# Kernel optimization log

Measured on AMD Instinct MI355X. Metric: run time of the kernel, lower is better.

Reference implementation:

```python
import jax, jax.numpy as jnp
import numpy as np

N, L, S, C, H = 4, 2048, 4096, 256, 8
D = C // H          # head dim = 32
HID = 4 * C         # mlp hidden = 1024
LN_EPS = 1e-5
LA_EPS = 1e-6


def _layer_norm(x, g, b):
    m = x.mean(-1, keepdims=True)
    v = ((x - m) ** 2).mean(-1, keepdims=True)
    return (x - m) * jax.lax.rsqrt(v + LN_EPS) * g + b


def _linear_attention(q, k, v):
    # q: [N,L,H,D], k/v: [N,S,H,D]  (elu feature map linear attention)
    Q = jax.nn.elu(q) + 1.0
    K = jax.nn.elu(k) + 1.0
    v_len = v.shape[1]
    KV = jnp.einsum('nshd,nshv->nhdv', K, v / v_len)
    Z = 1.0 / (jnp.einsum('nlhd,nhd->nlh', Q, K.sum(axis=1)) + LA_EPS)
    return jnp.einsum('nlhd,nhdv,nlh->nlhv', Q, KV, Z) * v_len


def setup_inputs() -> dict:
    key = jax.random.key(0)
    ks = jax.random.split(key, 32)
    f32 = jnp.float32
    w = lambda k, *s: (jax.random.normal(k, s, dtype=f32) * 0.02)
    inp = {
        'tgt': jax.random.normal(ks[0], (N, L, C), dtype=f32),
        'memory': jax.random.normal(ks[1], (N, S, C), dtype=f32),
        'tgt_pos': jax.random.normal(ks[2], (N, L, C), dtype=f32),
        'pos_embed': w(ks[3], 1, S, C),
        # layer norms
        'ln1_g': jnp.ones((C,), f32), 'ln1_b': jnp.zeros((C,), f32),
        'ln2_g': jnp.ones((C,), f32), 'ln2_b': jnp.zeros((C,), f32),
        'ln3_g': jnp.ones((C,), f32), 'ln3_b': jnp.zeros((C,), f32),
        # self-attn projections (stored (in,out))
        'wq': w(ks[4], C, C), 'bq': jnp.zeros((C,), f32),
        'wk': w(ks[5], C, C), 'bk': jnp.zeros((C,), f32),
        'wv': w(ks[6], C, C), 'bv': jnp.zeros((C,), f32),
        'w_merge': w(ks[7], C, C),
        # cross-attn (CCAttention) projections
        'cwq': w(ks[8], C, C), 'cbq': jnp.zeros((C,), f32),
        'cwk': w(ks[9], C, C), 'cbk': jnp.zeros((C,), f32),
        'cwv': w(ks[10], C, C), 'cbv': jnp.zeros((C,), f32),
        'cwo': w(ks[11], C, C), 'cbo': jnp.zeros((C,), f32),
        # mlp (fc1 -> dwconv3x3 -> gelu -> fc2)
        'mw1': w(ks[12], C, HID), 'mb1': jnp.zeros((HID,), f32),
        'dw_k': w(ks[13], HID, 1, 3, 3), 'dw_b': jnp.zeros((HID,), f32),
        'mw2': w(ks[14], HID, C), 'mb2': jnp.zeros((C,), f32),
        'num_points': L,
    }
    return inp


def reference(tgt, memory, tgt_pos, pos_embed,
              ln1_g, ln1_b, ln2_g, ln2_b, ln3_g, ln3_b,
              wq, bq, wk, bk, wv, bv, w_merge,
              cwq, cbq, cwk, cbk, cwv, cbv, cwo, cbo,
              mw1, mb1, dw_k, dw_b, mw2, mb2, num_points):
    n, l, c = tgt.shape
    # ---- self attention (linear attention) ----
    tgt2 = _layer_norm(tgt, ln1_g, ln1_b)
    qk = tgt2 + tgt_pos
    q = (qk @ wq + bq).reshape(n, l, H, D)
    k = (qk @ wk + bk).reshape(n, l, H, D)
    v = (tgt2 @ wv + bv).reshape(n, l, H, D)
    msg = _linear_attention(q, k, v).reshape(n, l, c) @ w_merge
    tgt = tgt + msg  # dropout is identity in eval
    # ---- cross attention (CCAttention, softmax MHA) ----
    tgt2 = _layer_norm(tgt, ln2_g, ln2_b)
    mem = memory + pos_embed
    cq = (tgt2 @ cwq + cbq).reshape(n, l, H, D)
    ck = (mem @ cwk + cbk).reshape(n, -1, H, D)
    cv = (mem @ cwv + cbv).reshape(n, -1, H, D)
    scale = D ** -0.5
    attn = jax.nn.softmax(jnp.einsum('nlhd,nshd->nhls', cq, ck) * scale, axis=-1)
    cmsg = jnp.einsum('nhls,nshd->nlhd', attn, cv).reshape(n, l, c) @ cwo + cbo
    tgt = tgt + cmsg
    # ---- MLP with depthwise conv over (num_points, 1) grid ----
    x = _layer_norm(tgt, ln3_g, ln3_b)
    h = x @ mw1 + mb1                                   # [n,l,HID]
    hi = h.transpose(0, 2, 1).reshape(n, HID, num_points, 1)
    hi = jax.lax.conv_general_dilated(
        hi, dw_k, window_strides=(1, 1), padding=((1, 1), (1, 1)),
        feature_group_count=HID,
        dimension_numbers=('NCHW', 'OIHW', 'NCHW'))
    hi = hi + dw_b[None, :, None, None]
    h = hi.reshape(n, HID, l).transpose(0, 2, 1)
    h = jax.nn.gelu(h, approximate=False)
    mlp_out = h @ mw2 + mb2
    return tgt + mlp_out
```

## Files before the change

### kernel.cpp

```cpp
#include <hip/hip_runtime.h>
#include <hip/hip_bf16.h>
#include <math.h>

#define NB 4
#define LL 2048
#define SS 4096
#define CC 256
#define HH 8
#define DD 32
#define HIDN 1024
#define NSPLIT 2

using bf16 = __hip_bfloat16;
typedef __attribute__((ext_vector_type(8))) short short8;
typedef __attribute__((ext_vector_type(4))) short short4v;
typedef __attribute__((ext_vector_type(4))) float floatx4;

__device__ __forceinline__ float b2f(bf16 x) { return __bfloat162float(x); }
__device__ __forceinline__ short f2bs(float x) {
    bf16 h = __float2bfloat16(x);
    return *(short*)&h;
}
__device__ __forceinline__ short f2bs_fast(float x) {
    return (short)(__float_as_uint(x) >> 16);
}
__device__ __forceinline__ float s2f(short s) {
    bf16 h = *(bf16*)&s;
    return __bfloat162float(h);
}

#if __has_builtin(__builtin_amdgcn_exp2f)
#define EXP2(x) __builtin_amdgcn_exp2f(x)
#else
#define EXP2(x) exp2f(x)
#endif

__device__ __forceinline__ bool probe_f32(const unsigned* p) {
    return p[0] == 0x3F800000u;
}
__device__ __forceinline__ float ldx(const void* p, size_t i, bool f32m) {
    return f32m ? ((const float*)p)[i] : b2f(((const bf16*)p)[i]);
}

__global__ __launch_bounds__(256)
void zero_kernel(float* __restrict__ p, int n) {
    int i = blockIdx.x * 256 + threadIdx.x;
    if (i < n) p[i] = 0.0f;
}

struct WPack { const void* p[10]; };

__global__ __launch_bounds__(256)
void wprep_kernel(WPack pk, short* __restrict__ dst,
                  const unsigned* __restrict__ probe) {
    const bool f32m = probe_f32(probe);
    const int z = blockIdx.z;
    const int K = (z == 9) ? 1024 : 256;
    const int N = (z == 8) ? 1024 : 256;
    const size_t off = (z < 8) ? (size_t)z * 65536 : (z == 8 ? 524288u : 786432u);
    const int k0 = blockIdx.y * 64, n0 = blockIdx.x * 64;
    if (k0 >= K || n0 >= N) return;
    __shared__ float T[64][65];
    const void* src = pk.p[z];
    const int tid = threadIdx.x;
    #pragma unroll
    for (int p = 0; p < 16; ++p) {
        int idx = tid + p * 256;
        int r = idx >> 6, c = idx & 63;
        T[r][c] = ldx(src, (size_t)(k0 + r) * N + n0 + c, f32m);
    }
    __syncthreads();
    short* d = dst + off;
    #pragma unroll
    for (int p = 0; p < 16; ++p) {
        int idx = tid + p * 256;
        int c2 = idx >> 6, r2 = idx & 63;
        d[(size_t)(n0 + c2) * K + k0 + r2] = f2bs(T[r2][c2]);
    }
}

__global__ __launch_bounds__(256)
void ln_kernel(const void* __restrict__ xr, const float* __restrict__ xf,
               const void* __restrict__ g, const void* __restrict__ bta,
               const void* __restrict__ pos,
               short* __restrict__ y, short* __restrict__ y2,
               const unsigned* __restrict__ probe) {
    const bool f32m = probe_f32(probe);
    const int row = blockIdx.x;
    const int c = threadIdx.x;
    const size_t base = (size_t)row * CC;
    float x = xr ? ldx(xr, base + c, f32m) : xf[base + c];
    float a = x, b = x * x;
    #pragma unroll
    for (int off = 32; off; off >>= 1) {
        a += __shfl_down(a, off);
        b += __shfl_down(b, off);
    }
    __shared__ float sa[4], sb[4];
    if ((c & 63) == 0) { sa[c >> 6] = a; sb[c >> 6] = b; }
    __syncthreads();
    float s1 = sa[0] + sa[1] + sa[2] + sa[3];
    float s2 = sb[0] + sb[1] + sb[2] + sb[3];
    float mean = s1 * (1.0f / CC);
    float var = s2 * (1.0f / CC) - mean * mean;
    float inv = rsqrtf(var + 1e-5f);
    float yv = (x - mean) * inv * ldx(g, c, f32m) + ldx(bta, c, f32m);
    y[base + c] = f2bs(yv);
    if (y2) y2[base + c] = f2bs(yv + ldx(pos, base + c, f32m));
}

__global__ __launch_bounds__(256)
void addpos_kernel(const void* __restrict__ mem, const void* __restrict__ pos,
                   short* __restrict__ out, const unsigned* __restrict__ probe) {
    const bool f32m = probe_f32(probe);
    const int row = blockIdx.x;
    const int c = threadIdx.x;
    const int s = row & (SS - 1);
    out[(size_t)row * CC + c] =
        f2bs(ldx(mem, (size_t)row * CC + c, f32m) + ldx(pos, (size_t)s * CC + c, f32m));
}

template <int BM, int BN, int EPI, int OUTMODE, int TRANSC2>
__global__ __launch_bounds__(256)
void gemm_mfma_kernel(const short* __restrict__ A, const short* __restrict__ Bt,
                      const void* __restrict__ bias, const void* __restrict__ bias2,
                      const float* __restrict__ residF, const void* __restrict__ residR,
                      void* __restrict__ Cout, void* __restrict__ Cout2,
                      int M, int N, int K, const unsigned* __restrict__ probe) {
    const bool f32m = probe_f32(probe);
    constexpr int WM = BM / 2, AI = WM / 16;
    constexpr int WN = BN / 2, BJ = WN / 16;
    constexpr int ACH = (BM == 128) ? 4 : 2;
    constexpr int BCH = (BN == 128) ? 4 : 2;
    __shared__ __attribute__((aligned(16))) short As[BM][72];
    __shared__ __attribute__((aligned(16))) short Bs[BN][72];
    const int tid = threadIdx.x;
    const int ln = tid & 15, quad = (tid >> 4) & 3, w = tid >> 6;
    const int wm = (w & 1) * WM, wn = (w >> 1) * WN;
    const int bm = blockIdx.y * BM, bn = blockIdx.x * BN;
    const int ar = (BM == 128) ? (tid >> 1) : (tid >> 2);
    const int ac = (BM == 128) ? ((tid & 1) * 32) : ((tid & 3) * 16);
    const int br = (BN == 128) ? (tid >> 1) : (tid >> 2);
    const int bc = (BN == 128) ? ((tid & 1) * 32) : ((tid & 3) * 16);

    short8 pa[ACH], pb[BCH];
    {
        const short* ag = &A[(size_t)(bm + ar) * K + ac];
        #pragma unroll
        for (int t = 0; t < ACH; ++t) pa[t] = *(const short8*)(ag + t * 8);
        const short* bg = &Bt[(size_t)(bn + br) * K + bc];
        #pragma unroll
        for (int t = 0; t < BCH; ++t) pb[t] = *(const short8*)(bg + t * 8);
    }
    floatx4 acc[AI][BJ] = {};
    for (int k0 = 0; k0 < K; k0 += 64) {
        #pragma unroll
        for (int t = 0; t < ACH; ++t) *(short8*)&As[ar][ac + t * 8] = pa[t];
        #pragma unroll
        for (int t = 0; t < BCH; ++t) *(short8*)&Bs[br][bc + t * 8] = pb[t];
        if (k0 + 64 < K) {
            const short* ag = &A[(size_t)(bm + ar) * K + k0 + 64 + ac];
            #pragma unroll
            for (int t = 0; t < ACH; ++t) pa[t] = *(const short8*)(ag + t * 8);
            const short* bg = &Bt[(size_t)(bn + br) * K + k0 + 64 + bc];
            #pragma unroll
            for (int t = 0; t < BCH; ++t) pb[t] = *(const short8*)(bg + t * 8);
        }
        __syncthreads();
        #pragma unroll
        for (int ks = 0; ks < 2; ++ks) {
            short8 af[AI], bf[BJ];
            #pragma unroll
            for (int i = 0; i < AI; ++i)
                af[i] = *(const short8*)&As[wm + i * 16 + ln][ks * 32 + quad * 8];
            #pragma unroll
            for (int j = 0; j < BJ; ++j)
                bf[j] = *(const short8*)&Bs[wn + j * 16 + ln][ks * 32 + quad * 8];
            #pragma unroll
            for (int i = 0; i < AI; ++i)
                #pragma unroll
                for (int j = 0; j < BJ; ++j)
                    acc[i][j] = __builtin_amdgcn_mfma_f32_16x16x32_bf16(af[i], bf[j], acc[i][j], 0, 0, 0);
        }
        __syncthreads();
    }
    #pragma unroll
    for (int i = 0; i < AI; ++i)
        #pragma unroll
        for (int j = 0; j < BJ; ++j) {
            const int gr0 = bm + wm + i * 16 + quad * 4;
            const int gc = bn + wn + j * 16 + ln;
            const bool hi = (Cout2 != nullptr) && (gc >= 256);
            const int col = hi ? gc - 256 : gc;
            const int sN = Cout2 ? 256 : N;
            void* co = hi ? Cout2 : Cout;
            const void* bb = hi ? bias2 : bias;
            float vv[4];
            #pragma unroll
            for (int r = 0; r < 4; ++r) {
                float v = acc[i][j][r];
                if (bb) v += ldx(bb, col, f32m);
                if (EPI == 1) v = (v > 0.0f) ? (v + 1.0f) : __expf(v);
                const size_t o = (size_t)(gr0 + r) * sN + col;
                if (residF) v += residF[o];
                if (residR) v += ldx(residR, o, f32m);
                vv[r] = v;
            }
            if (TRANSC2 && hi) {
                const int nb = gr0 >> 12;
                const int s = gr0 & (SS - 1);
                short4v pk4 = {f2bs(vv[0]), f2bs(vv[1]), f2bs(vv[2]), f2bs(vv[3])};
                *(short4v*)&((short*)co)[((size_t)nb * CC + col) * SS + s] = pk4;
            } else {
                #pragma unroll
                for (int r = 0; r < 4; ++r) {
                    const size_t o = (size_t)(gr0 + r) * sN + col;
                    if (OUTMODE == 0) ((float*)co)[o] = vv[r];
                    else if (OUTMODE == 2) ((short*)co)[o] = f2bs(vv[r]);
                    else {
                        if (f32m) ((float*)co)[o] = vv[r];
                        else      ((bf16*)co)[o] = __float2bfloat16(vv[r]);
                    }
                }
            }
        }
}

#define KVSPLIT 16
__global__ __launch_bounds__(256)
void linattn_kv_kernel(const float* __restrict__ Kp, const float* __restrict__ Vp,
                       float* __restrict__ KV, float* __restrict__ Ksum) {
    const int h = blockIdx.x, n = blockIdx.y, z = blockIdx.z;
    __shared__ __attribute__((aligned(16))) float Kt[64][33];
    __shared__ __attribute__((aligned(16))) float Vt[64][32];
    const int tid = threadIdx.x;
    const int d = tid >> 3, e0 = (tid & 7) * 4;
    const int sbeg = z * (LL / KVSPLIT), send = sbeg + (LL / KVSPLIT);
    float acc[4] = {}, ks = 0.0f;
    for (int s0 = sbeg; s0 < send; s0 += 64) {
        #pragma unroll
        for (int p = 0; p < 8; ++p) {
            int idx = tid + p * 256;
            int r = idx >> 5, c = idx & 31;
            size_t gaddr = (size_t)((n * LL) + s0 + r) * CC + h * DD + c;
            Kt[r][c] = Kp[gaddr];
            Vt[r][c] = Vp[gaddr];
        }
        __syncthreads();
        for (int s = 0; s < 64; ++s) {
            float kd = Kt[s][d];
            ks += kd;
            float4 v4 = *(const float4*)&Vt[s][e0];
            acc[0] += kd * v4.x; acc[1] += kd * v4.y;
            acc[2] += kd * v4.z; acc[3] += kd * v4.w;
        }
        __syncthreads();
    }
    float* kvp = &KV[(size_t)((n * HH + h) * DD + d) * DD + e0];
    atomicAdd(&kvp[0], acc[0]); atomicAdd(&kvp[1], acc[1]);
    atomicAdd(&kvp[2], acc[2]); atomicAdd(&kvp[3], acc[3]);
    if ((tid & 7) == 0) atomicAdd(&Ksum[(n * HH + h) * DD + d], ks);
}

__global__ __launch_bounds__(256)
void linattn_out_kernel(const float* __restrict__ Qp, const float* __restrict__ KV,
                        const float* __restrict__ Ksum, short* __restrict__ Out) {
    const int lt = blockIdx.x, h = blockIdx.y, n = blockIdx.z;
    __shared__ float KVs[32][33];
    __shared__ float Ks[32];
    __shared__ float Qs[64][33];
    const int tid = threadIdx.x;
    for (int p = 0; p < 4; ++p) {
        int idx = tid + p * 256;
        KVs[idx >> 5][idx & 31] = KV[(size_t)(n * HH + h) * (DD * DD) + idx];
    }
    if (tid < 32) Ks[tid] = Ksum[(n * HH + h) * DD + tid];
    for (int p = 0; p < 8; ++p) {
        int idx = tid + p * 256;
        int r = idx >> 5, c = idx & 31;
        Qs[r][c] = Qp[(size_t)((n * LL) + lt * 64 + r) * CC + h * DD + c];
    }
    __syncthreads();
    const int e = tid & 31;
    for (int ii = 0; ii < 8; ++ii) {
        const int i = (tid >> 5) + ii * 8;
        float num = 0.0f, den = 0.0f;
        for (int d = 0; d < 32; ++d) {
            float q = Qs[i][d];
            num += q * KVs[d][e];
            den += q * Ks[d];
        }
        Out[(size_t)((n * LL) + lt * 64 + i) * CC + h * DD + e] = f2bs(num / (den + 1e-6f));
    }
}

__global__ __launch_bounds__(256)
void flash_mfma_kernel(const short* __restrict__ Q, const short* __restrict__ K,
                       const short* __restrict__ V,
                       float* __restrict__ Of, float* __restrict__ Lp) {
    const int lt = blockIdx.x, h = blockIdx.y;
    const int n = blockIdx.z >> 1, sp = blockIdx.z & 1;
    const int tid = threadIdx.x;
    const int ln = tid & 15;
    const int quad = (tid >> 4) & 3;
    const int w = tid >> 6;
    const int NT = NB * LL;
    const float qscale = 0.17677669529663687f * 1.4426950408889634f;

    __shared__ __attribute__((aligned(16))) short Qs[64][40];
    __shared__ __attribute__((aligned(16))) short Ks[2][64][40];
    __shared__ __attribute__((aligned(16))) short Vp[2][32][72];

    {
        const int r = tid >> 2, c0 = (tid & 3) * 8;
        short8 qv = *(const short8*)&Q[(size_t)((n * LL) + lt * 64 + r) * CC + h * DD + c0];
        short tmp[8];
        #pragma unroll
        for (int j = 0; j < 8; ++j) tmp[j] = f2bs(s2f(qv[j]) * qscale);
        *(short8*)&Qs[r][c0] = *(short8*)tmp;
    }
    __syncthreads();

    short8 bQ = *(const short8*)&Qs[w * 16 + ln][quad * 8];

    const short one_b = (short)0x3F80;
    const short8 ones8 = {one_b, one_b, one_b, one_b, one_b, one_b, one_b, one_b};

    floatx4 o0 = {0.f, 0.f, 0.f, 0.f};
    floatx4 o1 = {0.f, 0.f, 0.f, 0.f};
    floatx4 o2 = {0.f, 0.f, 0.f, 0.f};
    const floatx4 zinit = {-24.f, -24.f, -24.f, -24.f};

    const int r_st = tid >> 2, c0_st = (tid & 3) * 8;
    const int e_st = tid >> 3, m_st = tid & 7;
    const int K32 = (m_st >> 2) * 32;
    const int h4 = ((m_st >> 1) & 1) * 4;
    const int q0s = (2 * m_st) & 3;
    const int slotA = K32 + q0s * 8 + h4;
    const int slotB = K32 + (q0s + 1) * 8 + h4;

    const int sbeg = sp * (SS / NSPLIT);
    constexpr int NIT = (SS / NSPLIT) / 64;

    const short* kptr = &K[(size_t)((n * SS) + sbeg + r_st) * CC + h * DD + c0_st];
    const short* vptr = &V[((size_t)n * CC + h * DD + e_st) * SS + sbeg + m_st * 8];
    short8 kreg = *(const short8*)kptr;
    short8 vreg = *(const short8*)vptr;

    for (int it = 0; it < NIT; ++it) {
        const int buf = it & 1;
        *(short8*)&Ks[buf][r_st][c0_st] = kreg;
        {
            short4v lo = {vreg[0], vreg[1], vreg[2], vreg[3]};
            short4v hi = {vreg[4], vreg[5], vreg[6], vreg[7]};
            *(short4v*)&Vp[buf][e_st][slotA] = lo;
            *(short4v*)&Vp[buf][e_st][slotB] = hi;
        }
        if (it + 1 < NIT) {
            kreg = *(const short8*)(kptr + (size_t)(it + 1) * 64 * CC);
            vreg = *(const short8*)(vptr + (it + 1) * 64);
        }
        __syncthreads();

        floatx4 sc[4];
        #pragma unroll
        for (int g = 0; g < 4; ++g) {
            short8 aK = *(const short8*)&Ks[buf][g * 16 + ln][quad * 8];
            sc[g] = __builtin_amdgcn_mfma_f32_16x16x32_bf16(aK, bQ, zinit, 0, 0, 0);
        }

        #pragma unroll
        for (int ks = 0; ks < 2; ++ks) {
            union { unsigned u[4]; short8 s8; } cvt;
            #pragma unroll
            for (int jj = 0; jj < 4; ++jj) {
                const int j0 = 2 * jj, j1 = 2 * jj + 1;
                float p0 = EXP2(sc[2 * ks + (j0 >> 2)][j0 & 3]);
                float p1 = EXP2(sc[2 * ks + (j1 >> 2)][j1 & 3]);
                cvt.u[jj] = __builtin_amdgcn_perm(
                    __float_as_uint(p1), __float_as_uint(p0), 0x07060302u);
            }
            short8 aP = cvt.s8;
            short8 bV0 = *(const short8*)&Vp[buf][ln][ks * 32 + quad * 8];
            short8 bV1 = *(const short8*)&Vp[buf][16 + ln][ks * 32 + quad * 8];
            o0 = __builtin_amdgcn_mfma_f32_16x16x32_bf16(aP, bV0, o0, 0, 0, 0);
            o1 = __builtin_amdgcn_mfma_f32_16x16x32_bf16(aP, bV1, o1, 0, 0, 0);
            o2 = __builtin_amdgcn_mfma_f32_16x16x32_bf16(aP, ones8, o2, 0, 0, 0);
        }
    }

    const int rowbase = lt * 64 + w * 16;
    if (ln == 0) {
        #pragma unroll
        for (int r = 0; r < 4; ++r)
            Lp[((size_t)sp * NT + (size_t)n * LL + rowbase + quad * 4 + r) * HH + h] = o2[r];
    }
    #pragma unroll
    for (int r = 0; r < 4; ++r) {
        const size_t row = (size_t)n * LL + rowbase + quad * 4 + r;
        float* o = &Of[((size_t)sp * NT + row) * CC + h * DD];
        o[ln] = o0[r];
        o[16 + ln] = o1[r];
    }
}

__global__ __launch_bounds__(256)
void flash_merge_kernel(const float* __restrict__ Of, const float* __restrict__ Lp,
                        short* __restrict__ O) {
    const int row = blockIdx.x, c = threadIdx.x, h = c >> 5;
    const size_t NT = (size_t)NB * LL;
    float l = Lp[(size_t)row * HH + h] + Lp[(NT + row) * HH + h];
    float v = Of[(size_t)row * CC + c] + Of[NT * CC + (size_t)row * CC + c];
    O[(size_t)row * CC + c] = f2bs(v / l);
}

__global__ __launch_bounds__(256)
void dwconv_gelu_kernel(const short* __restrict__ H1, const void* __restrict__ wk,
                        const void* __restrict__ wb, short* __restrict__ H2,
                        const unsigned* __restrict__ probe) {
    const bool f32m = probe_f32(probe);
    const int row = blockIdx.x;
    const int l = row & (LL - 1);
    const int c0 = threadIdx.x * 4;
    const short* cur = &H1[(size_t)row * HIDN + c0];
    short4v xc = *(const short4v*)cur;
    short4v xm = {}, xp = {};
    if (l > 0)      xm = *(const short4v*)(cur - HIDN);
    if (l < LL - 1) xp = *(const short4v*)(cur + HIDN);
    short r[4];
    #pragma unroll
    for (int j = 0; j < 4; ++j) {
        int ch = c0 + j;
        float wm = ldx(wk, ch * 9 + 1, f32m);
        float w0 = ldx(wk, ch * 9 + 4, f32m);
        float wp = ldx(wk, ch * 9 + 7, f32m);
        float v = s2f(xm[j]) * wm + s2f(xc[j]) * w0 + s2f(xp[j]) * wp + ldx(wb, ch, f32m);
        r[j] = f2bs(0.5f * v * (1.0f + erff(v * 0.70710678118654752f)));
    }
    short4v out = {r[0], r[1], r[2], r[3]};
    *(short4v*)&H2[(size_t)row * HIDN + c0] = out;
}

extern "C" void kernel_launch(void* const* d_in, const int* in_sizes, int n_in,
                              void* d_out, int out_size, void* d_ws, size_t ws_size,
                              hipStream_t stream) {
    const void* tgt      = d_in[0];
    const void* memory   = d_in[1];
    const void* tgt_pos  = d_in[2];
    const void* pos_emb  = d_in[3];
    const void* ln1_g = d_in[4],  *ln1_b = d_in[5];
    const void* ln2_g = d_in[6],  *ln2_b = d_in[7];
    const void* ln3_g = d_in[8],  *ln3_b = d_in[9];
    const void* wq = d_in[10], *bq = d_in[11];
    const void* wk = d_in[12], *bk = d_in[13];
    const void* wv = d_in[14], *bv = d_in[15];
    const void* w_merge = d_in[16];
    const void* cwq = d_in[17], *cbq = d_in[18];
    const void* cwk = d_in[19], *cbk = d_in[20];
    const void* cwv = d_in[21], *cbv = d_in[22];
    const void* cwo = d_in[23], *cbo = d_in[24];
    const void* mw1 = d_in[25], *mb1 = d_in[26];
    const void* dw_k = d_in[27], *dw_b = d_in[28];
    const void* mw2 = d_in[29], *mb2 = d_in[30];
    const unsigned* probe = (const unsigned*)d_in[4];

    char* w = (char*)d_ws;
    const size_t MB = 1024 * 1024;
    short* lnout_b = (short*)(w + 0 * MB);
    short* qk_b    = (short*)(w + 4 * MB);
    float* Tbuf    = (float*)(w + 8 * MB);
    float* phiq    = (float*)(w + 16 * MB);
    float* phik    = (float*)(w + 24 * MB);
    float* vbuf    = (float*)(w + 32 * MB);
    float* KVb     = (float*)(w + 40 * MB);
    float* Ksb     = (float*)(w + 40 * MB + 131072);
    short* cqbuf   = (short*)(w + 41 * MB);
    short* membuf  = (short*)(w + 45 * MB);
    short* ckbuf   = (short*)(w + 53 * MB);
    short* cvT     = (short*)(w + 69 * MB);
    short* flashO  = (short*)(w + 77 * MB);
    short* wT      = (short*)(w + 81 * MB);
    float* Ofb     = (float*)(w + 16 * MB);
    float* Lpb     = (float*)(w + 32 * MB);
    short* H1      = (short*)(w + 16 * MB);
    short* H2      = (short*)(w + 32 * MB);

    short* wqT  = wT + 0 * 65536;
    short* wvT  = wT + 2 * 65536;
    short* wmT  = wT + 3 * 65536;
    short* cwqT = wT + 4 * 65536;
    short* cwkT = wT + 5 * 65536;
    short* cwoT = wT + 7 * 65536;
    short* mw1T = wT + 524288;
    short* mw2T = wT + 786432;

    const int NT = NB * LL;
    const int NS = NB * SS;
    const dim3 blk(256);

    WPack pk;
    pk.p[0] = wq;  pk.p[1] = wk;  pk.p[2] = wv;  pk.p[3] = w_merge;
    pk.p[4] = cwq; pk.p[5] = cwk; pk.p[6] = cwv; pk.p[7] = cwo;
    pk.p[8] = mw1; pk.p[9] = mw2;
    wprep_kernel<<<dim3(16, 16, 10), blk, 0, stream>>>(pk, wT, probe);
    zero_kernel<<<dim3(137), blk, 0, stream>>>(KVb, 35072);

    ln_kernel<<<NT, blk, 0, stream>>>(tgt, nullptr, ln1_g, ln1_b, tgt_pos, lnout_b, qk_b, probe);
    gemm_mfma_kernel<64, 64, 1, 0, 0><<<dim3(8, NT / 64), blk, 0, stream>>>(
        qk_b, wqT, bq, bk, nullptr, nullptr, phiq, phik, NT, 512, CC, probe);
    gemm_mfma_kernel<64, 64, 0, 0, 0><<<dim3(4, NT / 64), blk, 0, stream>>>(
        lnout_b, wvT, bv, nullptr, nullptr, nullptr, vbuf, nullptr, NT, CC, CC, probe);
    linattn_kv_kernel<<<dim3(HH, NB, KVSPLIT), blk, 0, stream>>>(phik, vbuf, KVb, Ksb);
    linattn_out_kernel<<<dim3(LL / 64, HH, NB), blk, 0, stream>>>(phiq, KVb, Ksb, (short*)vbuf);
    gemm_mfma_kernel<64, 64, 0, 0, 0><<<dim3(4, NT / 64), blk, 0, stream>>>(
        (short*)vbuf, wmT, nullptr, nullptr, nullptr, tgt, Tbuf, nullptr, NT, CC, CC, probe);

    ln_kernel<<<NT, blk, 0, stream>>>(nullptr, Tbuf, ln2_g, ln2_b, nullptr, lnout_b, nullptr, probe);
    addpos_kernel<<<NS, blk, 0, stream>>>(memory, pos_emb, membuf, probe);
    gemm_mfma_kernel<64, 64, 0, 2, 0><<<dim3(4, NT / 64), blk, 0, stream>>>(
        lnout_b, cwqT, cbq, nullptr, nullptr, nullptr, cqbuf, nullptr, NT, CC, CC, probe);
    gemm_mfma_kernel<64, 64, 0, 2, 1><<<dim3(8, NS / 64), blk, 0, stream>>>(
        membuf, cwkT, cbk, cbv, nullptr, nullptr, ckbuf, cvT, NS, 512, CC, probe);
    flash_mfma_kernel<<<dim3(LL / 64, HH, NB * NSPLIT), blk, 0, stream>>>(
        cqbuf, ckbuf, cvT, Ofb, Lpb);
    flash_merge_kernel<<<NT, blk, 0, stream>>>(Ofb, Lpb, flashO);
    gemm_mfma_kernel<64, 64, 0, 0, 0><<<dim3(4, NT / 64), blk, 0, stream>>>(
        flashO, cwoT, cbo, nullptr, Tbuf, nullptr, Tbuf, nullptr, NT, CC, CC, probe);

    ln_kernel<<<NT, blk, 0, stream>>>(nullptr, Tbuf, ln3_g, ln3_b, nullptr, lnout_b, nullptr, probe);
    gemm_mfma_kernel<64, 64, 0, 2, 0><<<dim3(16, NT / 64), blk, 0, stream>>>(
        lnout_b, mw1T, mb1, nullptr, nullptr, nullptr, H1, nullptr, NT, HIDN, CC, probe);
    dwconv_gelu_kernel<<<NT, blk, 0, stream>>>(H1, dw_k, dw_b, H2, probe);
    gemm_mfma_kernel<64, 64, 0, 1, 0><<<dim3(4, NT / 64), blk, 0, stream>>>(
        H2, mw2T, mb2, nullptr, Tbuf, nullptr, d_out, nullptr, NT, CC, HIDN, probe);

    (void)in_sizes; (void)n_in; (void)out_size; (void)ws_size;
}
```

Measured before the change: 428.7 us.

## Process 128 query rows per flash block and fold zeroing into wprep

The cross-attention flash kernel now handles two 64-row query tiles per block. Each K/V tile loaded into shared memory is reused for twice as many queries, which halves global K/V traffic and barrier count per query row. The grid shrinks to 16x8x8=1024 blocks, and register pressure rises from the doubled accumulators and score tiles. Separately, the KV buffer zeroing launch is merged into the weight-prep kernel as an extra z-slice, removing one kernel launch.

```diff
diff --git a/kernel.cpp b/kernel.cpp
--- a/kernel.cpp
+++ b/kernel.cpp
@@ -42,19 +42,19 @@
     return f32m ? ((const float*)p)[i] : b2f(((const bf16*)p)[i]);
 }
 
-__global__ __launch_bounds__(256)
-void zero_kernel(float* __restrict__ p, int n) {
-    int i = blockIdx.x * 256 + threadIdx.x;
-    if (i < n) p[i] = 0.0f;
-}
-
 struct WPack { const void* p[10]; };
 
 __global__ __launch_bounds__(256)
-void wprep_kernel(WPack pk, short* __restrict__ dst,
+void wprep_kernel(WPack pk, short* __restrict__ dst, float* __restrict__ zbuf,
                   const unsigned* __restrict__ probe) {
+    const int z = blockIdx.z;
+    const int tid = threadIdx.x;
+    if (z == 10) {
+        int idx = (blockIdx.y * 16 + blockIdx.x) * 256 + tid;
+        if (idx < 35072) zbuf[idx] = 0.0f;
+        return;
+    }
     const bool f32m = probe_f32(probe);
-    const int z = blockIdx.z;
     const int K = (z == 9) ? 1024 : 256;
     const int N = (z == 8) ? 1024 : 256;
     const size_t off = (z < 8) ? (size_t)z * 65536 : (z == 8 ? 524288u : 786432u);
@@ -62,7 +62,6 @@
     if (k0 >= K || n0 >= N) return;
     __shared__ float T[64][65];
     const void* src = pk.p[z];
-    const int tid = threadIdx.x;
     #pragma unroll
     for (int p = 0; p < 16; ++p) {
         int idx = tid + p * 256;
@@ -307,28 +306,34 @@
     const int NT = NB * LL;
     const float qscale = 0.17677669529663687f * 1.4426950408889634f;
 
-    __shared__ __attribute__((aligned(16))) short Qs[64][40];
+    __shared__ __attribute__((aligned(16))) short Qs[128][40];
     __shared__ __attribute__((aligned(16))) short Ks[2][64][40];
     __shared__ __attribute__((aligned(16))) short Vp[2][32][72];
 
     {
         const int r = tid >> 2, c0 = (tid & 3) * 8;
-        short8 qv = *(const short8*)&Q[(size_t)((n * LL) + lt * 64 + r) * CC + h * DD + c0];
-        short tmp[8];
-        #pragma unroll
-        for (int j = 0; j < 8; ++j) tmp[j] = f2bs(s2f(qv[j]) * qscale);
-        *(short8*)&Qs[r][c0] = *(short8*)tmp;
+        #pragma unroll
+        for (int hf = 0; hf < 2; ++hf) {
+            short8 qv = *(const short8*)
+                &Q[(size_t)((n * LL) + lt * 128 + hf * 64 + r) * CC + h * DD + c0];
+            short tmp[8];
+            #pragma unroll
+            for (int j = 0; j < 8; ++j) tmp[j] = f2bs(s2f(qv[j]) * qscale);
+            *(short8*)&Qs[hf * 64 + r][c0] = *(short8*)tmp;
+        }
     }
     __syncthreads();
 
-    short8 bQ = *(const short8*)&Qs[w * 16 + ln][quad * 8];
+    short8 bQa = *(const short8*)&Qs[w * 16 + ln][quad * 8];
+    short8 bQb = *(const short8*)&Qs[64 + w * 16 + ln][quad * 8];
 
     const short one_b = (short)0x3F80;
     const short8 ones8 = {one_b, one_b, one_b, one_b, one_b, one_b, one_b, one_b};
 
-    floatx4 o0 = {0.f, 0.f, 0.f, 0.f};
-    floatx4 o1 = {0.f, 0.f, 0.f, 0.f};
-    floatx4 o2 = {0.f, 0.f, 0.f, 0.f};
+    floatx4 o0a = {0.f, 0.f, 0.f, 0.f}, o1a = {0.f, 0.f, 0.f, 0.f};
+    floatx4 o2a = {0.f, 0.f, 0.f, 0.f};
+    floatx4 o0b = {0.f, 0.f, 0.f, 0.f}, o1b = {0.f, 0.f, 0.f, 0.f};
+    floatx4 o2b = {0.f, 0.f, 0.f, 0.f};
     const floatx4 zinit = {-24.f, -24.f, -24.f, -24.f};
 
     const int r_st = tid >> 2, c0_st = (tid & 3) * 8;
@@ -362,45 +367,63 @@
         }
         __syncthreads();
 
-        floatx4 sc[4];
+        floatx4 sa[4], sb[4];
         #pragma unroll
         for (int g = 0; g < 4; ++g) {
             short8 aK = *(const short8*)&Ks[buf][g * 16 + ln][quad * 8];
-            sc[g] = __builtin_amdgcn_mfma_f32_16x16x32_bf16(aK, bQ, zinit, 0, 0, 0);
+            sa[g] = __builtin_amdgcn_mfma_f32_16x16x32_bf16(aK, bQa, zinit, 0, 0, 0);
+            sb[g] = __builtin_amdgcn_mfma_f32_16x16x32_bf16(aK, bQb, zinit, 0, 0, 0);
         }
 
         #pragma unroll
         for (int ks = 0; ks < 2; ++ks) {
-            union { unsigned u[4]; short8 s8; } cvt;
+            union { unsigned u[4]; short8 s8; } ca, cb;
             #pragma unroll
             for (int jj = 0; jj < 4; ++jj) {
                 const int j0 = 2 * jj, j1 = 2 * jj + 1;
-                float p0 = EXP2(sc[2 * ks + (j0 >> 2)][j0 & 3]);
-                float p1 = EXP2(sc[2 * ks + (j1 >> 2)][j1 & 3]);
-                cvt.u[jj] = __builtin_amdgcn_perm(
-                    __float_as_uint(p1), __float_as_uint(p0), 0x07060302u);
+                float pa0 = EXP2(sa[2 * ks + (j0 >> 2)][j0 & 3]);
+                float pa1 = EXP2(sa[2 * ks + (j1 >> 2)][j1 & 3]);
+                ca.u[jj] = __builtin_amdgcn_perm(
+                    __float_as_uint(pa1), __float_as_uint(pa0), 0x07060302u);
+                float pb0 = EXP2(sb[2 * ks + (j0 >> 2)][j0 & 3]);
+                float pb1 = EXP2(sb[2 * ks + (j1 >> 2)][j1 & 3]);
+                cb.u[jj] = __builtin_amdgcn_perm(
+                    __float_as_uint(pb1), __float_as_uint(pb0), 0x07060302u);
             }
-            short8 aP = cvt.s8;
             short8 bV0 = *(const short8*)&Vp[buf][ln][ks * 32 + quad * 8];
             short8 bV1 = *(const short8*)&Vp[buf][16 + ln][ks * 32 + quad * 8];
-            o0 = __builtin_amdgcn_mfma_f32_16x16x32_bf16(aP, bV0, o0, 0, 0, 0);
-            o1 = __builtin_amdgcn_mfma_f32_16x16x32_bf16(aP, bV1, o1, 0, 0, 0);
-            o2 = __builtin_amdgcn_mfma_f32_16x16x32_bf16(aP, ones8, o2, 0, 0, 0);
-        }
-    }
-
-    const int rowbase = lt * 64 + w * 16;
+            o0a = __builtin_amdgcn_mfma_f32_16x16x32_bf16(ca.s8, bV0, o0a, 0, 0, 0);
+            o1a = __builtin_amdgcn_mfma_f32_16x16x32_bf16(ca.s8, bV1, o1a, 0, 0, 0);
+            o2a = __builtin_amdgcn_mfma_f32_16x16x32_bf16(ca.s8, ones8, o2a, 0, 0, 0);
+            o0b = __builtin_amdgcn_mfma_f32_16x16x32_bf16(cb.s8, bV0, o0b, 0, 0, 0);
+            o1b = __builtin_amdgcn_mfma_f32_16x16x32_bf16(cb.s8, bV1, o1b, 0, 0, 0);
+            o2b = __builtin_amdgcn_mfma_f32_16x16x32_bf16(cb.s8, ones8, o2b, 0, 0, 0);
+        }
+    }
+
+    const int rb_a = lt * 128 + w * 16;
+    const int rb_b = rb_a + 64;
     if (ln == 0) {
         #pragma unroll
-        for (int r = 0; r < 4; ++r)
-            Lp[((size_t)sp * NT + (size_t)n * LL + rowbase + quad * 4 + r) * HH + h] = o2[r];
+        for (int r = 0; r < 4; ++r) {
+            Lp[((size_t)sp * NT + (size_t)n * LL + rb_a + quad * 4 + r) * HH + h] = o2a[r];
+            Lp[((size_t)sp * NT + (size_t)n * LL + rb_b + quad * 4 + r) * HH + h] = o2b[r];
+        }
     }
     #pragma unroll
     for (int r = 0; r < 4; ++r) {
-        const size_t row = (size_t)n * LL + rowbase + quad * 4 + r;
-        float* o = &Of[((size_t)sp * NT + row) * CC + h * DD];
-        o[ln] = o0[r];
-        o[16 + ln] = o1[r];
+        {
+            const size_t row = (size_t)n * LL + rb_a + quad * 4 + r;
+            float* o = &Of[((size_t)sp * NT + row) * CC + h * DD];
+            o[ln] = o0a[r];
+            o[16 + ln] = o1a[r];
+        }
+        {
+            const size_t row = (size_t)n * LL + rb_b + quad * 4 + r;
+            float* o = &Of[((size_t)sp * NT + row) * CC + h * DD];
+            o[ln] = o0b[r];
+            o[16 + ln] = o1b[r];
+        }
     }
 }
 
@@ -502,8 +525,7 @@
     pk.p[0] = wq;  pk.p[1] = wk;  pk.p[2] = wv;  pk.p[3] = w_merge;
     pk.p[4] = cwq; pk.p[5] = cwk; pk.p[6] = cwv; pk.p[7] = cwo;
     pk.p[8] = mw1; pk.p[9] = mw2;
-    wprep_kernel<<<dim3(16, 16, 10), blk, 0, stream>>>(pk, wT, probe);
-    zero_kernel<<<dim3(137), blk, 0, stream>>>(KVb, 35072);
+    wprep_kernel<<<dim3(16, 16, 11), blk, 0, stream>>>(pk, wT, KVb, probe);
 
     ln_kernel<<<NT, blk, 0, stream>>>(tgt, nullptr, ln1_g, ln1_b, tgt_pos, lnout_b, qk_b, probe);
     gemm_mfma_kernel<64, 64, 1, 0, 0><<<dim3(8, NT / 64), blk, 0, stream>>>(
@@ -521,7 +543,7 @@
         lnout_b, cwqT, cbq, nullptr, nullptr, nullptr, cqbuf, nullptr, NT, CC, CC, probe);
     gemm_mfma_kernel<64, 64, 0, 2, 1><<<dim3(8, NS / 64), blk, 0, stream>>>(
         membuf, cwkT, cbk, cbv, nullptr, nullptr, ckbuf, cvT, NS, 512, CC, probe);
-    flash_mfma_kernel<<<dim3(LL / 64, HH, NB * NSPLIT), blk, 0, stream>>>(
+    flash_mfma_kernel<<<dim3(LL / 128, HH, NB * NSPLIT), blk, 0, stream>>>(
         cqbuf, ckbuf, cvT, Ofb, Lpb);
     flash_merge_kernel<<<NT, blk, 0, stream>>>(Ofb, Lpb, flashO);
     gemm_mfma_kernel<64, 64, 0, 0, 0><<<dim3(4, NT / 64), blk, 0, stream>>>(
```

Result: no change. 421.0 us (-1.8%).
